# Optimization experiments

Measured on AMD Instinct MI355X. Metric: run time of the kernel, lower is better.

Reference implementation:

```python
import jax, jax.numpy as jnp
import numpy as np

N = 16384
IN = 64
H = 128
OUT = 64
K = 32


def setup_inputs() -> dict:
    key = jax.random.key(0)
    ks = jax.random.split(key, 5)

    def unif(k, shape):
        fan_in = shape[1]
        std = 1.0 / np.sqrt(fan_in)
        return jax.random.uniform(k, shape, jnp.float32, -std, std)

    x = jax.random.normal(ks[0], (N, IN), jnp.float32)
    w0 = unif(ks[1], (H, 2 * IN))            # layer 0: in_dim = 64
    w2_0 = unif(ks[2], (OUT, IN + H))
    in1 = IN + OUT                            # dense concat: 128
    w1 = unif(ks[3], (H, 2 * in1))
    w2_1 = unif(ks[4], (OUT, in1 + H))
    return {"x": x, "w0": w0, "w2_0": w2_0, "w1": w1, "w2_1": w2_1}


def _affinity_kernel(x, w, w2, k):
    # kNN graph via squared Euclidean distances (monotone in torch.norm)
    sq = jnp.sum(x * x, axis=1)
    d2 = sq[:, None] + sq[None, :] - 2.0 * (x @ x.T)   # (N, N)
    _, idx = jax.lax.top_k(-d2, k)                      # k smallest distances, (N, k)
    nbr = x[idx]                                        # (N, k, D) gather
    self_b = jnp.broadcast_to(x[:, None, :], nbr.shape)
    cat = jnp.concatenate([nbr, self_b], axis=-1)       # (N, k, 2D)
    h = jnp.einsum('nkd,hd->nkh', cat, w)
    h = jnp.clip(h, -1.0, 1.0)                          # Hardtanh
    pooled = h.mean(axis=1)                             # average pooling, (N, H)
    return jnp.concatenate([pooled, x], axis=-1) @ w2.T  # (N, out_dim)


def reference(x, w0, w2_0, w1, w2_1):
    o0 = _affinity_kernel(x, w0, w2_0, K)
    x1 = jnp.concatenate([x, o0], axis=-1)   # dense connectivity (forward_input=True)
    o1 = _affinity_kernel(x1, w1, w2_1, K)
    return o1
```

## Files before the change

kernel.cpp:

```cpp
#include <hip/hip_runtime.h>
#include <hip/hip_bf16.h>

#define NP   16384
#define KNN  32
#define HDIM 128
#define ODIM 64

typedef __attribute__((ext_vector_type(8))) short bf16x8;
typedef __attribute__((ext_vector_type(4))) float f32x4;

__global__ __launch_bounds__(256)
void split_kernel(const float* __restrict__ X, unsigned short* __restrict__ hi,
                  unsigned short* __restrict__ lo, int n4) {
    const int i = blockIdx.x * 256 + threadIdx.x;
    if (i >= n4) return;
    const float4 v = reinterpret_cast<const float4*>(X)[i];
    const float vv[4] = {v.x, v.y, v.z, v.w};
    ushort4 h, l;
    unsigned short* hp = &h.x;
    unsigned short* lp = &l.x;
    #pragma unroll
    for (int c = 0; c < 4; ++c) {
        __hip_bfloat16 hb = __float2bfloat16(vv[c]);
        const float hf = __bfloat162float(hb);
        __hip_bfloat16 lb = __float2bfloat16(vv[c] - hf);
        hp[c] = *reinterpret_cast<unsigned short*>(&hb);
        lp[c] = *reinterpret_cast<unsigned short*>(&lb);
    }
    reinterpret_cast<ushort4*>(hi)[i] = h;
    reinterpret_cast<ushort4*>(lo)[i] = l;
}

__global__ __launch_bounds__(256)
void wsplit_kernel(const float* __restrict__ W, unsigned short* __restrict__ hi,
                   unsigned short* __restrict__ lo, int Dd) {
    const int i = blockIdx.x * 256 + threadIdx.x;
    if (i >= HDIM * Dd) return;
    const int hh = i / Dd, d = i % Dd;
    const float v = W[(size_t)hh * (2 * Dd) + d];
    __hip_bfloat16 hb = __float2bfloat16(v);
    const float hf = __bfloat162float(hb);
    __hip_bfloat16 lb = __float2bfloat16(v - hf);
    hi[i] = *reinterpret_cast<unsigned short*>(&hb);
    lo[i] = *reinterpret_cast<unsigned short*>(&lb);
}

template<int D>
__global__ __launch_bounds__(256)
void sq_kernel(const float* __restrict__ X, float* __restrict__ sq) {
    const int lane = threadIdx.x & 63;
    const int row  = blockIdx.x * 4 + (threadIdx.x >> 6);
    float s = 0.f;
    #pragma unroll
    for (int d = lane; d < D; d += 64) {
        const float v = X[(size_t)row * D + d];
        s = fmaf(v, v, s);
    }
    #pragma unroll
    for (int off = 32; off; off >>= 1) s += __shfl_down(s, off);
    if (lane == 0) sq[row] = s;
}

template<int D>
__global__ __launch_bounds__(512, 4)
void topk_kernel(const unsigned short* __restrict__ Xhi,
                 const unsigned short* __restrict__ Xlo,
                 const float* __restrict__ sq, int* __restrict__ topIdx) {
    constexpr int TI = 16, JC = 128, SS = JC + 1;
    constexpr int NT = NP / JC;
    constexpr int KQ = D / 8;
    constexpr int KS = D / 32;
    constexpr int PLSLOT = JC * KQ;
    constexpr int CALLS = 2 * PLSLOT / 512;
    __shared__ __align__(16) unsigned short xjB[2 * PLSLOT * 8];
    __shared__ float scoresR[TI * SS];

    const int t = threadIdx.x;
    const int lane = t & 63;
    const int waveU = __builtin_amdgcn_readfirstlane(t >> 6);
    const int rowBase = blockIdx.x * TI;
    const int l15 = lane & 15, l4 = lane >> 4;
    const float INF = __builtin_inff();
    const int jcol = 16 * waveU + l15;

    bf16x8 Ahi[KS], Alo[KS];
    #pragma unroll
    for (int s = 0; s < KS; ++s) {
        const size_t off = (size_t)(rowBase + l15) * D + 32 * s + 8 * l4;
        Ahi[s] = *reinterpret_cast<const bf16x8*>(Xhi + off);
        Alo[s] = *reinterpret_cast<const bf16x8*>(Xlo + off);
    }

    float tv[2]; int tidx[2]; float minv[2];
    #pragma unroll
    for (int r = 0; r < 2; ++r) { tv[r] = -INF; tidx[r] = 0x7fffffff; minv[r] = -INF; }

    auto stageTile = [&](int jb) {
        #pragma unroll
        for (int c = 0; c < CALLS; ++c) {
            const int slotBase = (waveU * CALLS + c) * 64;
            const int sl = slotBase + lane;
            const int pl = sl / PLSLOT;
            const int ps = sl % PLSLOT;
            const int j  = ps / KQ;
            const int kq = (ps % KQ) ^ (j & (KQ - 1));
            const unsigned short* src =
                (pl ? Xlo : Xhi) + (size_t)(jb + j) * D + 8 * kq;
            __builtin_amdgcn_global_load_lds(
                (const __attribute__((address_space(1))) void*)src,
                (__attribute__((address_space(3))) void*)&xjB[(size_t)slotBase * 8],
                16, 0, 0);
        }
    };

    stageTile(0);
    __syncthreads();

    for (int it = 0; it < NT; ++it) {
        const int jb = it * JC;
        const float sub0 = 0.5f * sq[jb + lane];
        const float sub1 = 0.5f * sq[jb + 64 + lane];

        f32x4 Ca = {0,0,0,0}, Cb = {0,0,0,0}, Cc = {0,0,0,0};
        #pragma unroll
        for (int s = 0; s < KS; ++s) {
            const int kq = 4 * s + l4;
            const int slot = jcol * KQ + (kq ^ (jcol & (KQ - 1)));
            const bf16x8 Bh = *reinterpret_cast<const bf16x8*>(&xjB[(size_t)slot * 8]);
            const bf16x8 Bl = *reinterpret_cast<const bf16x8*>(&xjB[(size_t)(PLSLOT + slot) * 8]);
            Ca = __builtin_amdgcn_mfma_f32_16x16x32_bf16(Ahi[s], Bh, Ca, 0, 0, 0);
            Cb = __builtin_amdgcn_mfma_f32_16x16x32_bf16(Ahi[s], Bl, Cb, 0, 0, 0);
            Cc = __builtin_amdgcn_mfma_f32_16x16x32_bf16(Alo[s], Bh, Cc, 0, 0, 0);
        }
        #pragma unroll
        for (int r = 0; r < 4; ++r)
            scoresR[(4 * l4 + r) * SS + jcol] = (Ca[r] + Cb[r]) + Cc[r];
        __syncthreads();

        if (it + 1 < NT) stageTile(jb + JC);

        #pragma unroll
        for (int h = 0; h < 2; ++h) {
            float sv[2];
            unsigned long long m[2];
            #pragma unroll
            for (int r = 0; r < 2; ++r) {
                sv[r] = scoresR[(2 * waveU + r) * SS + h * 64 + lane]
                      - (h ? sub1 : sub0);
                m[r] = __ballot(sv[r] > minv[r]);
            }
            while (m[0] | m[1]) {
                #pragma unroll
                for (int r = 0; r < 2; ++r) {
                    if (m[r]) {
                        const int l = __builtin_ctzll(m[r]);
                        m[r] &= m[r] - 1;
                        const float cv = __shfl(sv[r], l);
                        const int   cj = jb + h * 64 + l;
                        const float upv = __shfl_up(tv[r], 1);
                        const int   upi = __shfl_up(tidx[r], 1);
                        const bool ge = (lane < KNN) && (tv[r] >= cv);
                        const int p = __popcll(__ballot(ge));
                        if (lane == p)                   { tv[r] = cv;  tidx[r] = cj; }
                        else if (lane > p && lane < KNN) { tv[r] = upv; tidx[r] = upi; }
                    }
                }
            }
        }
        #pragma unroll
        for (int r = 0; r < 2; ++r)
            minv[r] = __shfl(tv[r], KNN - 1);

        __syncthreads();
    }

    if (lane < KNN) {
        #pragma unroll
        for (int r = 0; r < 2; ++r)
            topIdx[(size_t)(rowBase + waveU * 2 + r) * KNN + lane] = tidx[r];
    }
}

template<int D, int LAYER>
__global__ __launch_bounds__(512, 4)
void mlp_kernel(const float* __restrict__ X,
                const unsigned short* __restrict__ Xhi,
                const unsigned short* __restrict__ Xlo,
                const unsigned short* __restrict__ WAhi,
                const unsigned short* __restrict__ WAlo,
                const float* __restrict__ W, const float* __restrict__ W2,
                const int* __restrict__ topIdx, float* __restrict__ out) {
    constexpr int RPB = 2;
    constexpr int KS = D / 32;
    constexpr int W2C  = HDIM + D;
    constexpr int SPL2 = 4;
    constexpr int CL   = W2C / SPL2;
    __shared__ float AT[D * HDIM];
    __shared__ float xi[RPB][D];
    __shared__ float hself_s[RPB][HDIM];
    __shared__ float part[RPB][2][HDIM];
    __shared__ int   idx_s[RPB][KNN];

    const int t = threadIdx.x;
    const int lane = t & 63;
    const int waveU = __builtin_amdgcn_readfirstlane(t >> 6);
    const int rowBase = blockIdx.x * RPB;
    const int l15 = lane & 15, l4 = lane >> 4;

    if (t < RPB * D / 4) {
        const int i = t / (D / 4), dg = t % (D / 4);
        const float4 v = *reinterpret_cast<const float4*>(
            X + (size_t)(rowBase + i) * D + 4 * dg);
        xi[i][4 * dg + 0] = v.x; xi[i][4 * dg + 1] = v.y;
        xi[i][4 * dg + 2] = v.z; xi[i][4 * dg + 3] = v.w;
    }
    if (t < RPB * KNN)
        idx_s[t >> 5][t & 31] = topIdx[(size_t)(rowBase + (t >> 5)) * KNN + (t & 31)];
    bf16x8 Ahi[KS], Alo[KS];
    #pragma unroll
    for (int s = 0; s < KS; ++s) {
        const size_t off = (size_t)(waveU * 16 + l15) * D + 32 * s + 8 * l4;
        Ahi[s] = *reinterpret_cast<const bf16x8*>(WAhi + off);
        Alo[s] = *reinterpret_cast<const bf16x8*>(WAlo + off);
    }
    for (int e = t; e < HDIM * D / 4; e += 512) {
        const int hh = e % HDIM, dg = e / HDIM;
        const float4 v = *reinterpret_cast<const float4*>(
            W + (size_t)hh * (2 * D) + D + 4 * dg);
        AT[(4 * dg + 0) * HDIM + hh] = v.x; AT[(4 * dg + 1) * HDIM + hh] = v.y;
        AT[(4 * dg + 2) * HDIM + hh] = v.z; AT[(4 * dg + 3) * HDIM + hh] = v.w;
    }
    __syncthreads();

    if (t < RPB * HDIM) {
        const int row = t >> 7, hh = t & 127;
        float s = 0.f;
        #pragma unroll 8
        for (int d = 0; d < D; ++d)
            s = fmaf(AT[d * HDIM + hh], xi[row][d], s);
        hself_s[row][hh] = s;
    }
    __syncthreads();

    #pragma unroll
    for (int a = 0; a < 4; ++a) {
        const int row = a >> 1, kT = a & 1;
        const int nIdx = idx_s[row][kT * 16 + l15];
        bf16x8 Bh[KS], Bl[KS];
        #pragma unroll
        for (int s = 0; s < KS; ++s) {
            const size_t off = (size_t)nIdx * D + 32 * s + 8 * l4;
            Bh[s] = *reinterpret_cast<const bf16x8*>(Xhi + off);
            Bl[s] = *reinterpret_cast<const bf16x8*>(Xlo + off);
        }
        f32x4 Ca = {0,0,0,0}, Cb = {0,0,0,0}, Cc = {0,0,0,0};
        #pragma unroll
        for (int s = 0; s < KS; ++s) {
            Ca = __builtin_amdgcn_mfma_f32_16x16x32_bf16(Ahi[s], Bh[s], Ca, 0, 0, 0);
            Cb = __builtin_amdgcn_mfma_f32_16x16x32_bf16(Ahi[s], Bl[s], Cb, 0, 0, 0);
            Cc = __builtin_amdgcn_mfma_f32_16x16x32_bf16(Alo[s], Bh[s], Cc, 0, 0, 0);
        }
        float ps[4];
        #pragma unroll
        for (int r = 0; r < 4; ++r) {
            const float h = (Ca[r] + Cb[r]) + Cc[r]
                          + hself_s[row][waveU * 16 + 4 * l4 + r];
            ps[r] = fminf(1.f, fmaxf(-1.f, h));
        }
        #pragma unroll
        for (int off = 1; off <= 8; off <<= 1)
            #pragma unroll
            for (int r = 0; r < 4; ++r)
                ps[r] += __shfl_xor(ps[r], off);
        if (l15 == 0)
            #pragma unroll
            for (int r = 0; r < 4; ++r)
                part[row][kT][waveU * 16 + 4 * l4 + r] = ps[r] * (1.f / KNN);
    }
    __syncthreads();

    {
        const int og   = t / SPL2;
        const int spl  = t % SPL2;
        const int orow = og >> 6, o = og & 63;
        const int c0   = spl * CL;
        float s = 0.f;
        for (int c4 = 0; c4 < CL / 4; ++c4) {
            const int c = c0 + 4 * c4;
            const float4 w = *reinterpret_cast<const float4*>(W2 + (size_t)o * W2C + c);
            float vs[4];
            if (c < HDIM) {
                const float4 q0 = *reinterpret_cast<const float4*>(&part[orow][0][c]);
                const float4 q1 = *reinterpret_cast<const float4*>(&part[orow][1][c]);
                vs[0] = q0.x + q1.x; vs[1] = q0.y + q1.y;
                vs[2] = q0.z + q1.z; vs[3] = q0.w + q1.w;
            } else {
                const float4 xv = *reinterpret_cast<const float4*>(&xi[orow][c - HDIM]);
                vs[0] = xv.x; vs[1] = xv.y; vs[2] = xv.z; vs[3] = xv.w;
            }
            const float wv[4] = {w.x, w.y, w.z, w.w};
            #pragma unroll
            for (int j = 0; j < 4; ++j)
                s = fmaf(vs[j], wv[j], s);
        }
        #pragma unroll
        for (int off = SPL2 / 2; off; off >>= 1) s += __shfl_down(s, off);
        if (spl == 0) {
            if (LAYER == 0)
                out[(size_t)(rowBase + orow) * 128 + 64 + o] = s;
            else
                out[(size_t)(rowBase + orow) * ODIM + o] = s;
        }
    }
    if (LAYER == 0 && t < RPB * 64) {
        const int orow = t >> 6, d = t & 63;
        out[(size_t)(rowBase + orow) * 128 + d] = xi[orow][d];
    }
}

extern "C" void kernel_launch(void* const* d_in, const int* in_sizes, int n_in,
                              void* d_out, int out_size, void* d_ws, size_t ws_size,
                              hipStream_t stream) {
    const float* x    = (const float*)d_in[0];
    const float* w0   = (const float*)d_in[1];
    const float* w2_0 = (const float*)d_in[2];
    const float* w1   = (const float*)d_in[3];
    const float* w2_1 = (const float*)d_in[4];
    float* out = (float*)d_out;

    char* ws = (char*)d_ws;
    float* sq  = (float*)ws;
    int*   idx = (int*)(ws + (size_t)NP * 4);
    float* x1  = (float*)(ws + (size_t)NP * 4 + (size_t)NP * KNN * 4);
    unsigned short* xhi = (unsigned short*)(ws + (size_t)NP * 4
                          + (size_t)NP * KNN * 4 + (size_t)NP * HDIM * 4);
    unsigned short* xlo = xhi + (size_t)NP * HDIM;
    unsigned short* wa0hi = xlo + (size_t)NP * HDIM;
    unsigned short* wa0lo = wa0hi + HDIM * 64;
    unsigned short* wa1hi = wa0lo + HDIM * 64;
    unsigned short* wa1lo = wa1hi + HDIM * 128;

    wsplit_kernel<<<(HDIM * 64 + 255) / 256, 256, 0, stream>>>(w0, wa0hi, wa0lo, 64);
    wsplit_kernel<<<(HDIM * 128 + 255) / 256, 256, 0, stream>>>(w1, wa1hi, wa1lo, 128);

    split_kernel<<<NP * 64 / 4 / 256, 256, 0, stream>>>(x, xhi, xlo, NP * 64 / 4);
    sq_kernel<64><<<NP / 4, 256, 0, stream>>>(x, sq);
    topk_kernel<64><<<NP / 16, 512, 0, stream>>>(xhi, xlo, sq, idx);
    mlp_kernel<64, 0><<<NP / 2, 512, 0, stream>>>(x, xhi, xlo, wa0hi, wa0lo,
                                                  w0, w2_0, idx, x1);

    split_kernel<<<NP * 128 / 4 / 256, 256, 0, stream>>>(x1, xhi, xlo, NP * 128 / 4);
    sq_kernel<128><<<NP / 4, 256, 0, stream>>>(x1, sq);
    topk_kernel<128><<<NP / 16, 512, 0, stream>>>(xhi, xlo, sq, idx);
    mlp_kernel<128, 1><<<NP / 2, 512, 0, stream>>>(x1, xhi, xlo, wa1hi, wa1lo,
                                                   w1, w2_1, idx, out);
}
```

Baseline: 1.972 ms.

## Process 32 query rows per topk block, reusing each staged column tile

The kNN top-k kernel now handles two 16-row query sub-blocks per workgroup, so every column tile staged into LDS feeds twice as many MFMA products and the number of workgroups is halved. The score buffer is reused for the two sub-blocks in turn, separated by extra barriers. Plain __syncthreads are replaced with explicit waitcnt plus s_barrier macros, and the broadcast of the candidate value uses readlane instead of shfl. The cost is higher register use for the second A fragment set, four running top-k lists per wave, more barriers per tile, and fewer blocks to spread across the GPU.

Measured after the change: 2.228 ms. 13.0% more time.

```diff
diff --git a/kernel.cpp b/kernel.cpp
--- a/kernel.cpp
+++ b/kernel.cpp
@@ -8,6 +8,17 @@
 
 typedef __attribute__((ext_vector_type(8))) short bf16x8;
 typedef __attribute__((ext_vector_type(4))) float f32x4;
+
+#define BAR_LGKM() do { \
+    asm volatile("s_waitcnt lgkmcnt(0)" ::: "memory"); \
+    __builtin_amdgcn_sched_barrier(0); \
+    __builtin_amdgcn_s_barrier(); \
+    __builtin_amdgcn_sched_barrier(0); } while (0)
+#define BAR_ALL() do { \
+    asm volatile("s_waitcnt vmcnt(0) lgkmcnt(0)" ::: "memory"); \
+    __builtin_amdgcn_sched_barrier(0); \
+    __builtin_amdgcn_s_barrier(); \
+    __builtin_amdgcn_sched_barrier(0); } while (0)
 
 __global__ __launch_bounds__(256)
 void split_kernel(const float* __restrict__ X, unsigned short* __restrict__ hi,
@@ -66,14 +77,14 @@
 void topk_kernel(const unsigned short* __restrict__ Xhi,
                  const unsigned short* __restrict__ Xlo,
                  const float* __restrict__ sq, int* __restrict__ topIdx) {
-    constexpr int TI = 16, JC = 128, SS = JC + 1;
+    constexpr int TI = 32, JC = 128, SS = JC + 1;
     constexpr int NT = NP / JC;
     constexpr int KQ = D / 8;
     constexpr int KS = D / 32;
     constexpr int PLSLOT = JC * KQ;
     constexpr int CALLS = 2 * PLSLOT / 512;
     __shared__ __align__(16) unsigned short xjB[2 * PLSLOT * 8];
-    __shared__ float scoresR[TI * SS];
+    __shared__ float scoresR[16 * SS];
 
     const int t = threadIdx.x;
     const int lane = t & 63;
@@ -83,17 +94,19 @@
     const float INF = __builtin_inff();
     const int jcol = 16 * waveU + l15;
 
-    bf16x8 Ahi[KS], Alo[KS];
-    #pragma unroll
-    for (int s = 0; s < KS; ++s) {
-        const size_t off = (size_t)(rowBase + l15) * D + 32 * s + 8 * l4;
-        Ahi[s] = *reinterpret_cast<const bf16x8*>(Xhi + off);
-        Alo[s] = *reinterpret_cast<const bf16x8*>(Xlo + off);
-    }
-
-    float tv[2]; int tidx[2]; float minv[2];
-    #pragma unroll
-    for (int r = 0; r < 2; ++r) { tv[r] = -INF; tidx[r] = 0x7fffffff; minv[r] = -INF; }
+    bf16x8 Ahi[2][KS], Alo[2][KS];
+    #pragma unroll
+    for (int rb = 0; rb < 2; ++rb)
+        #pragma unroll
+        for (int s = 0; s < KS; ++s) {
+            const size_t off = (size_t)(rowBase + rb * 16 + l15) * D + 32 * s + 8 * l4;
+            Ahi[rb][s] = *reinterpret_cast<const bf16x8*>(Xhi + off);
+            Alo[rb][s] = *reinterpret_cast<const bf16x8*>(Xlo + off);
+        }
+
+    float tv[4]; int tidx[4]; float minv[4];
+    #pragma unroll
+    for (int r = 0; r < 4; ++r) { tv[r] = -INF; tidx[r] = 0x7fffffff; minv[r] = -INF; }
 
     auto stageTile = [&](int jb) {
         #pragma unroll
@@ -113,72 +126,89 @@
         }
     };
 
+#define SCAN_PHASE(BASE, JB) do {                                              \
+    _Pragma("unroll")                                                          \
+    for (int h = 0; h < 2; ++h) {                                              \
+        float sv[2];                                                           \
+        unsigned long long m[2];                                               \
+        _Pragma("unroll")                                                      \
+        for (int r = 0; r < 2; ++r) {                                          \
+            sv[r] = scoresR[(2 * waveU + r) * SS + h * 64 + lane]              \
+                  - (h ? sub1 : sub0);                                         \
+            m[r] = __ballot(sv[r] > minv[(BASE) + r]);                         \
+        }                                                                      \
+        while (m[0] | m[1]) {                                                  \
+            _Pragma("unroll")                                                  \
+            for (int r = 0; r < 2; ++r) {                                      \
+                if (m[r]) {                                                    \
+                    const int l = __builtin_ctzll(m[r]);                       \
+                    m[r] &= m[r] - 1;                                          \
+                    const float cv = __int_as_float(                           \
+                        __builtin_amdgcn_readlane(__float_as_int(sv[r]), l));  \
+                    const int cj = (JB) + h * 64 + l;                          \
+                    const float upv = __shfl_up(tv[(BASE) + r], 1);            \
+                    const int   upi = __shfl_up(tidx[(BASE) + r], 1);          \
+                    const bool ge = (lane < KNN) && (tv[(BASE) + r] >= cv);    \
+                    const int pp = __popcll(__ballot(ge));                     \
+                    if (lane == pp) { tv[(BASE)+r] = cv;  tidx[(BASE)+r] = cj; } \
+                    else if (lane > pp && lane < KNN)                          \
+                                    { tv[(BASE)+r] = upv; tidx[(BASE)+r] = upi; } \
+                }                                                              \
+            }                                                                  \
+        }                                                                      \
+        minv[(BASE) + 0] = __shfl(tv[(BASE) + 0], KNN - 1);                    \
+        minv[(BASE) + 1] = __shfl(tv[(BASE) + 1], KNN - 1);                    \
+    } } while (0)
+
     stageTile(0);
-    __syncthreads();
+    BAR_ALL();
 
     for (int it = 0; it < NT; ++it) {
         const int jb = it * JC;
         const float sub0 = 0.5f * sq[jb + lane];
         const float sub1 = 0.5f * sq[jb + 64 + lane];
 
-        f32x4 Ca = {0,0,0,0}, Cb = {0,0,0,0}, Cc = {0,0,0,0};
+        f32x4 C0a = {0,0,0,0}, C0b = {0,0,0,0};
+        f32x4 C1a = {0,0,0,0}, C1b = {0,0,0,0};
         #pragma unroll
         for (int s = 0; s < KS; ++s) {
             const int kq = 4 * s + l4;
             const int slot = jcol * KQ + (kq ^ (jcol & (KQ - 1)));
             const bf16x8 Bh = *reinterpret_cast<const bf16x8*>(&xjB[(size_t)slot * 8]);
             const bf16x8 Bl = *reinterpret_cast<const bf16x8*>(&xjB[(size_t)(PLSLOT + slot) * 8]);
-            Ca = __builtin_amdgcn_mfma_f32_16x16x32_bf16(Ahi[s], Bh, Ca, 0, 0, 0);
-            Cb = __builtin_amdgcn_mfma_f32_16x16x32_bf16(Ahi[s], Bl, Cb, 0, 0, 0);
-            Cc = __builtin_amdgcn_mfma_f32_16x16x32_bf16(Alo[s], Bh, Cc, 0, 0, 0);
-        }
+            C0a = __builtin_amdgcn_mfma_f32_16x16x32_bf16(Ahi[0][s], Bh, C0a, 0, 0, 0);
+            C0b = __builtin_amdgcn_mfma_f32_16x16x32_bf16(Ahi[0][s], Bl, C0b, 0, 0, 0);
+            C0b = __builtin_amdgcn_mfma_f32_16x16x32_bf16(Alo[0][s], Bh, C0b, 0, 0, 0);
+            C1a = __builtin_amdgcn_mfma_f32_16x16x32_bf16(Ahi[1][s], Bh, C1a, 0, 0, 0);
+            C1b = __builtin_amdgcn_mfma_f32_16x16x32_bf16(Ahi[1][s], Bl, C1b, 0, 0, 0);
+            C1b = __builtin_amdgcn_mfma_f32_16x16x32_bf16(Alo[1][s], Bh, C1b, 0, 0, 0);
+        }
+
         #pragma unroll
         for (int r = 0; r < 4; ++r)
-            scoresR[(4 * l4 + r) * SS + jcol] = (Ca[r] + Cb[r]) + Cc[r];
-        __syncthreads();
-
+            scoresR[(4 * l4 + r) * SS + jcol] = C0a[r] + C0b[r];
+        BAR_LGKM();
         if (it + 1 < NT) stageTile(jb + JC);
-
-        #pragma unroll
-        for (int h = 0; h < 2; ++h) {
-            float sv[2];
-            unsigned long long m[2];
+        SCAN_PHASE(0, jb);
+        BAR_LGKM();
+
+        #pragma unroll
+        for (int r = 0; r < 4; ++r)
+            scoresR[(4 * l4 + r) * SS + jcol] = C1a[r] + C1b[r];
+        BAR_LGKM();
+        SCAN_PHASE(2, jb);
+        BAR_ALL();
+    }
+
+    if (lane < KNN) {
+        #pragma unroll
+        for (int p = 0; p < 2; ++p)
             #pragma unroll
-            for (int r = 0; r < 2; ++r) {
-                sv[r] = scoresR[(2 * waveU + r) * SS + h * 64 + lane]
-                      - (h ? sub1 : sub0);
-                m[r] = __ballot(sv[r] > minv[r]);
-            }
-            while (m[0] | m[1]) {
-                #pragma unroll
-                for (int r = 0; r < 2; ++r) {
-                    if (m[r]) {
-                        const int l = __builtin_ctzll(m[r]);
-                        m[r] &= m[r] - 1;
-                        const float cv = __shfl(sv[r], l);
-                        const int   cj = jb + h * 64 + l;
-                        const float upv = __shfl_up(tv[r], 1);
-                        const int   upi = __shfl_up(tidx[r], 1);
-                        const bool ge = (lane < KNN) && (tv[r] >= cv);
-                        const int p = __popcll(__ballot(ge));
-                        if (lane == p)                   { tv[r] = cv;  tidx[r] = cj; }
-                        else if (lane > p && lane < KNN) { tv[r] = upv; tidx[r] = upi; }
-                    }
-                }
-            }
-        }
-        #pragma unroll
-        for (int r = 0; r < 2; ++r)
-            minv[r] = __shfl(tv[r], KNN - 1);
-
-        __syncthreads();
-    }
-
-    if (lane < KNN) {
-        #pragma unroll
-        for (int r = 0; r < 2; ++r)
-            topIdx[(size_t)(rowBase + waveU * 2 + r) * KNN + lane] = tidx[r];
-    }
+            for (int r = 0; r < 2; ++r)
+                topIdx[(size_t)(rowBase + p * 16 + 2 * waveU + r) * KNN + lane]
+                    = tidx[p * 2 + r];
+    }
+#undef SCAN_PHASE
 }
 
 template<int D, int LAYER>
@@ -345,13 +375,13 @@
 
     split_kernel<<<NP * 64 / 4 / 256, 256, 0, stream>>>(x, xhi, xlo, NP * 64 / 4);
     sq_kernel<64><<<NP / 4, 256, 0, stream>>>(x, sq);
-    topk_kernel<64><<<NP / 16, 512, 0, stream>>>(xhi, xlo, sq, idx);
+    topk_kernel<64><<<NP / 32, 512, 0, stream>>>(xhi, xlo, sq, idx);
     mlp_kernel<64, 0><<<NP / 2, 512, 0, stream>>>(x, xhi, xlo, wa0hi, wa0lo,
                                                   w0, w2_0, idx, x1);
 
     split_kernel<<<NP * 128 / 4 / 256, 256, 0, stream>>>(x1, xhi, xlo, NP * 128 / 4);
     sq_kernel<128><<<NP / 4, 256, 0, stream>>>(x1, sq);
-    topk_kernel<128><<<NP / 16, 512, 0, stream>>>(xhi, xlo, sq, idx);
+    topk_kernel<128><<<NP / 32, 512, 0, stream>>>(xhi, xlo, sq, idx);
     mlp_kernel<128, 1><<<NP / 2, 512, 0, stream>>>(x1, xhi, xlo, wa1hi, wa1lo,
                                                    w1, w2_1, idx, out);
 }
```
